# Optimization experiments

Measured on AMD Instinct MI355X. Metric: run time of the kernel, lower is better.

The kernel has to match this reference:

```python
import jax, jax.numpy as jnp
import numpy as np

WINDOW_LENGTH = 8  # hop size used by overlap_and_add (matches init_kwargs)


def overlap_and_add(x, step):
    """x: [B, C, T, L] frames; returns [B, C, (T-1)*step + L].
    Requires L % step == 0 (standard Conv-TasNet overlap_and_add)."""
    B, C, T, L = x.shape
    k = L // step  # subframes per frame
    sub = x.reshape(B, C, T * k, step)
    # subframe j of frame t lands at output subframe t + j
    seg = (jnp.arange(T)[:, None] + jnp.arange(k)[None, :]).reshape(-1)
    out = jnp.zeros((B, C, T + k - 1, step), x.dtype).at[:, :, seg].add(sub)
    return out.reshape(B, C, (T + k - 1) * step)


def setup_inputs() -> dict:
    key = jax.random.key(0)
    k1, k2 = jax.random.split(key)
    B, C, D, T = 8, 2, 16, 128000
    x = jax.random.normal(k1, (B, C, D, T), dtype=jnp.float32)
    x_wave = jax.random.normal(k2, (B, D, T), dtype=jnp.float32)
    return {"x": x, "x_wave": x_wave, "pad_left": 8, "pad_right": 8}


def reference(x, x_wave, pad_left, pad_right):
    # x: [B, C, D, T] masks; x_wave: [B, D, T] encoder output
    x = x * x_wave[:, None]              # broadcast over speaker axis C
    x = jnp.transpose(x, (0, 1, 3, 2))   # [B, C, T, D] -> frames of length D
    y = overlap_and_add(x, WINDOW_LENGTH)  # [B, C, (T-1)*hop + D]
    if pad_right:
        y = y[:, :, pad_left:y.shape[-1] - pad_right]
    else:
        y = y[:, :, pad_left:]
    return y
```

## Files before the change

### kernel.cpp

```cpp
#include <hip/hip_runtime.h>


constexpr int B = 8;
constexpr int C = 2;
constexpr int D = 16;
constexpr int T = 128000;

__global__ __launch_bounds__(256) void oaa_seg_kernel(
    const float* __restrict__ x,
    const float* __restrict__ xw,
    float* __restrict__ out,
    int S)
{
    const int tid = blockIdx.x * 256 + threadIdx.x;
    const int seg = tid + 1;
    if (seg >= T) return;
    const int b = blockIdx.y;

    const float* xwb = xw + (size_t)b * (D * T);
    const float* xb  = x  + (size_t)b * (C * D * T);

    const int t0 = seg;
    const int t1 = seg - 1;

    float acc0[8], acc1[8];
#pragma unroll
    for (int d = 0; d < 8; ++d) {
        const float w0 = xwb[d * T + t0];
        const float w1 = xwb[(d + 8) * T + t1];
        acc0[d] = xb[d * T + t0] * w0
                + xb[(d + 8) * T + t1] * w1;
        acc1[d] = xb[(D + d) * T + t0] * w0
                + xb[(D + d + 8) * T + t1] * w1;
    }

    const size_t ob = (size_t)b * C * S;
    const int s0 = seg * 8 - 8;
    float4* o0 = (float4*)(out + ob + s0);
    float4* o1 = (float4*)(out + ob + S + s0);
    o0[0] = make_float4(acc0[0], acc0[1], acc0[2], acc0[3]);
    o0[1] = make_float4(acc0[4], acc0[5], acc0[6], acc0[7]);
    o1[0] = make_float4(acc1[0], acc1[1], acc1[2], acc1[3]);
    o1[1] = make_float4(acc1[4], acc1[5], acc1[6], acc1[7]);
}

extern "C" void kernel_launch(void* const* d_in, const int* in_sizes, int n_in,
                              void* d_out, int out_size, void* d_ws, size_t ws_size,
                              hipStream_t stream) {
    const float* x  = (const float*)d_in[0];
    const float* xw = (const float*)d_in[1];
    float* out = (float*)d_out;

    const int S = out_size / (B * C);
    const int nthreads = T - 1;
    const int nblk = (nthreads + 255) / 256;
    dim3 grid(nblk, B);
    oaa_seg_kernel<<<grid, dim3(256), 0, stream>>>(x, xw, out, S);
}
```

Measured before the change: 253.4 us.

## Stage masked products in LDS with vectorized loads and coalesced stores

Each block now loads a 256-frame tile of x and x_wave with float4 loads, multiplies them, and stores the products in a padded shared-memory tile, including a small halo from the previous tile. Threads then read the tile back and emit contiguous float4 output writes for the overlap-add. The aim is wider, better-coalesced global traffic in place of scalar strided loads and scattered stores. In exchange it adds a block barrier and shared-memory use, which may limit occupancy.

```diff
diff --git a/kernel.cpp b/kernel.cpp
--- a/kernel.cpp
+++ b/kernel.cpp
@@ -6,42 +6,74 @@
 constexpr int D = 16;
 constexpr int T = 128000;
 
-__global__ __launch_bounds__(256) void oaa_seg_kernel(
+constexpr int SEGS  = 256;
+constexpr int PITCH = 260;
+constexpr int NBLK  = T / SEGS;
+
+__global__ __launch_bounds__(256, 4) void oaa_lds_kernel(
     const float* __restrict__ x,
     const float* __restrict__ xw,
     float* __restrict__ out,
     int S)
 {
-    const int tid = blockIdx.x * 256 + threadIdx.x;
-    const int seg = tid + 1;
-    if (seg >= T) return;
-    const int b = blockIdx.y;
+    __shared__ float P[C][D][PITCH];
 
-    const float* xwb = xw + (size_t)b * (D * T);
-    const float* xb  = x  + (size_t)b * (C * D * T);
+    const int j  = threadIdx.x;
+    const int b  = blockIdx.y;
+    const int s0 = blockIdx.x * SEGS;
 
-    const int t0 = seg;
-    const int t1 = seg - 1;
+    const float* __restrict__ xwb = xw + (size_t)b * D * T;
+    const float* __restrict__ xb0 = x  + (size_t)b * C * D * T;
+    const float* __restrict__ xb1 = xb0 + (size_t)D * T;
 
-    float acc0[8], acc1[8];
 #pragma unroll
-    for (int d = 0; d < 8; ++d) {
-        const float w0 = xwb[d * T + t0];
-        const float w1 = xwb[(d + 8) * T + t1];
-        acc0[d] = xb[d * T + t0] * w0
-                + xb[(d + 8) * T + t1] * w1;
-        acc1[d] = xb[(D + d) * T + t0] * w0
-                + xb[(D + d + 8) * T + t1] * w1;
+    for (int i = 0; i < 4; ++i) {
+        const int tau = j + 256 * i;
+        const int d   = tau >> 6;
+        const int col = tau & 63;
+        const size_t g = (size_t)d * T + (size_t)(s0 + 4 * col);
+        const float4 wv  = *(const float4*)(xwb + g);
+        const float4 xv0 = *(const float4*)(xb0 + g);
+        const float4 xv1 = *(const float4*)(xb1 + g);
+        *(float4*)&P[0][d][4 + 4 * col] =
+            make_float4(xv0.x * wv.x, xv0.y * wv.y, xv0.z * wv.z, xv0.w * wv.w);
+        *(float4*)&P[1][d][4 + 4 * col] =
+            make_float4(xv1.x * wv.x, xv1.y * wv.y, xv1.z * wv.z, xv1.w * wv.w);
     }
+    if (j < 8) {
+        const int d  = j + 8;
+        const int th = (s0 >= 4) ? (s0 - 4) : 0;
+        const size_t g = (size_t)d * T + (size_t)th;
+        const float4 wv  = *(const float4*)(xwb + g);
+        const float4 xv0 = *(const float4*)(xb0 + g);
+        const float4 xv1 = *(const float4*)(xb1 + g);
+        *(float4*)&P[0][d][0] =
+            make_float4(xv0.x * wv.x, xv0.y * wv.y, xv0.z * wv.z, xv0.w * wv.w);
+        *(float4*)&P[1][d][0] =
+            make_float4(xv1.x * wv.x, xv1.y * wv.y, xv1.z * wv.z, xv1.w * wv.w);
+    }
+    __syncthreads();
 
     const size_t ob = (size_t)b * C * S;
-    const int s0 = seg * 8 - 8;
-    float4* o0 = (float4*)(out + ob + s0);
-    float4* o1 = (float4*)(out + ob + S + s0);
-    o0[0] = make_float4(acc0[0], acc0[1], acc0[2], acc0[3]);
-    o0[1] = make_float4(acc0[4], acc0[5], acc0[6], acc0[7]);
-    o1[0] = make_float4(acc1[0], acc1[1], acc1[2], acc1[3]);
-    o1[1] = make_float4(acc1[4], acc1[5], acc1[6], acc1[7]);
+#pragma unroll
+    for (int i = 0; i < 4; ++i) {
+        const int sig  = j + 256 * i;
+        const int half = sig & 1;
+        const int sloc = (sig >> 1) & (SEGS - 1);
+        const int c    = sig >> 9;
+        const int seg  = s0 + sloc;
+        if (seg != 0) {
+            const int dbase = 4 * half;
+            const int ta = sloc + 4;
+            const int tb = sloc + 3;
+            float4 o;
+            o.x = P[c][dbase + 0][ta] + P[c][dbase +  8][tb];
+            o.y = P[c][dbase + 1][ta] + P[c][dbase +  9][tb];
+            o.z = P[c][dbase + 2][ta] + P[c][dbase + 10][tb];
+            o.w = P[c][dbase + 3][ta] + P[c][dbase + 11][tb];
+            *(float4*)(out + ob + (size_t)c * S + (size_t)seg * 8 - 8 + dbase) = o;
+        }
+    }
 }
 
 extern "C" void kernel_launch(void* const* d_in, const int* in_sizes, int n_in,
@@ -52,8 +84,6 @@
     float* out = (float*)d_out;
 
     const int S = out_size / (B * C);
-    const int nthreads = T - 1;
-    const int nblk = (nthreads + 255) / 256;
-    dim3 grid(nblk, B);
-    oaa_seg_kernel<<<grid, dim3(256), 0, stream>>>(x, xw, out, S);
+    dim3 grid(NBLK, B);
+    oaa_lds_kernel<<<grid, dim3(256), 0, stream>>>(x, xw, out, S);
 }
```

After: 251.3 us. Within noise of the previous version (-0.8%).
